# Kernel optimization log

Measured on AMD Instinct MI355X. Metric: run time of the kernel, lower is better.

## Reference

```python
import jax, jax.numpy as jnp
import numpy as np
import math

EMBED_DIM = 768
NUM_HEADS = 12
SEQ_LEN = 2048
NUM_BLOCKS = 8
BLOCK_SIZE = EMBED_DIM // NUM_BLOCKS  # 96
HEAD_DIM = EMBED_DIM // NUM_HEADS     # 64
BATCH = 4


def build_sparse_mask(T):
    # local window of 5 (j in [i-4, i]) plus log-stride links at i-8, i-16, ...
    m = np.full((T, T), -np.inf, dtype=np.float32)
    for i in range(T):
        for j in range(max(0, i - 4), i + 1):
            m[i, j] = 0.0
        step = 8
        while i - step >= 0:
            m[i, i - step] = 0.0
            step *= 2
    return jnp.asarray(m)


def make_urdhva_params(key):
    k1, k2, k3 = jax.random.split(key, 3)
    s = BLOCK_SIZE ** 0.5
    Wv = jax.random.normal(k1, (NUM_BLOCKS, BLOCK_SIZE, BLOCK_SIZE), jnp.float32) / s
    Wr = jax.random.normal(k2, (NUM_BLOCKS - 1, BLOCK_SIZE, BLOCK_SIZE), jnp.float32) / s
    Wl = jax.random.normal(k3, (NUM_BLOCKS - 1, BLOCK_SIZE, BLOCK_SIZE), jnp.float32) / s
    b = jnp.zeros((EMBED_DIM,), jnp.float32)
    return Wv, Wr, Wl, b


def urdhva_linear(x, Wv, Wr, Wl, b):
    # x: [..., EMBED_DIM] -> block-diagonal + neighbor cross-block linear
    shp = x.shape
    xb = x.reshape(-1, NUM_BLOCKS, BLOCK_SIZE)  # [N, B, S]
    y = jnp.einsum('nbs,bst->nbt', xb, Wv)
    y = y.at[:, 1:, :].add(jnp.einsum('nbs,bst->nbt', xb[:, :-1, :], Wr))
    y = y.at[:, :-1, :].add(jnp.einsum('nbs,bst->nbt', xb[:, 1:, :], Wl))
    return y.reshape(shp) + b


def setup_inputs() -> dict:
    key = jax.random.key(0)
    kx, kq, kk, kv, ko = jax.random.split(key, 5)
    inp = {'x': jax.random.normal(kx, (BATCH, SEQ_LEN, EMBED_DIM), jnp.float32)}
    for name, k in (('q', kq), ('k', kk), ('v', kv), ('o', ko)):
        Wv, Wr, Wl, b = make_urdhva_params(k)
        inp[name + '_Wv'] = Wv
        inp[name + '_Wr'] = Wr
        inp[name + '_Wl'] = Wl
        inp[name + '_b'] = b
    inp['sparse_mask'] = build_sparse_mask(SEQ_LEN)
    return inp


def reference(x, q_Wv, q_Wr, q_Wl, q_b, k_Wv, k_Wr, k_Wl, k_b,
              v_Wv, v_Wr, v_Wl, v_b, o_Wv, o_Wr, o_Wl, o_b, sparse_mask):
    B, T, C = x.shape
    H, D = NUM_HEADS, HEAD_DIM
    q = urdhva_linear(x, q_Wv, q_Wr, q_Wl, q_b).reshape(B, T, H, D).transpose(0, 2, 1, 3)
    k = urdhva_linear(x, k_Wv, k_Wr, k_Wl, k_b).reshape(B, T, H, D).transpose(0, 2, 1, 3)
    v = urdhva_linear(x, v_Wv, v_Wr, v_Wl, v_b).reshape(B, T, H, D).transpose(0, 2, 1, 3)
    scores = jnp.einsum('bhqd,bhkd->bhqk', q, k) / math.sqrt(D)
    scores = scores + sparse_mask[:T, :T]
    attn = jax.nn.softmax(scores, axis=-1)
    out = jnp.einsum('bhqk,bhkd->bhqd', attn, v).transpose(0, 2, 1, 3).reshape(B, T, C)
    return urdhva_linear(out, o_Wv, o_Wr, o_Wl, o_b)
```

## Files before the change

kernel.cpp:

```cpp
#include <hip/hip_runtime.h>
#include <hip/hip_bf16.h>

typedef __hip_bfloat16 bf16;
typedef __attribute__((ext_vector_type(8))) short short8;
typedef __attribute__((ext_vector_type(4))) float f32x4;

#define ED 768
#define NB 8
#define BS 96
#define NH 12
#define HD 64
#define SEQ 2048
#define NBATCH 4
#define NROWS (NBATCH*SEQ)

__device__ __forceinline__ float b2f(bf16 v){ return __bfloat162float(v); }
__device__ __forceinline__ bf16 f2b(float v){ return __float2bfloat16(v); }
__device__ __forceinline__ short f2bs(float v){
    return (short)__builtin_bit_cast(unsigned short, __float2bfloat16(v));
}
__device__ __forceinline__ unsigned pkbf16(float lo, float hi){
    return (unsigned)(unsigned short)f2bs(lo) |
           ((unsigned)(unsigned short)f2bs(hi) << 16);
}
__device__ __forceinline__ void gload_lds16(const void* g, void* l) {
    __builtin_amdgcn_global_load_lds(
        (const __attribute__((address_space(1))) unsigned*)g,
        (__attribute__((address_space(3))) unsigned*)l, 16, 0, 0);
}

#define XCVT_BLKS (NROWS*ED/8/256)
#define DENS_BLKS (ED*ED/256)
__global__ __launch_bounds__(256) void prep(
    const float* __restrict__ x, bf16* __restrict__ xb,
    const float* __restrict__ qWv, const float* __restrict__ qWr, const float* __restrict__ qWl,
    const float* __restrict__ kWv, const float* __restrict__ kWr, const float* __restrict__ kWl,
    const float* __restrict__ vWv, const float* __restrict__ vWr, const float* __restrict__ vWl,
    const float* __restrict__ oWv, const float* __restrict__ oWr, const float* __restrict__ oWl,
    bf16* __restrict__ WdBase)
{
    if (blockIdx.x < XCVT_BLKS) {
        const int idx = blockIdx.x*256 + threadIdx.x;
        const float4 a = ((const float4*)x)[(size_t)idx*2];
        const float4 c = ((const float4*)x)[(size_t)idx*2 + 1];
        short8 o;
        o[0]=f2bs(a.x); o[1]=f2bs(a.y); o[2]=f2bs(a.z); o[3]=f2bs(a.w);
        o[4]=f2bs(c.x); o[5]=f2bs(c.y); o[6]=f2bs(c.z); o[7]=f2bs(c.w);
        ((short8*)xb)[idx] = o;
    } else {
        const int bid = blockIdx.x - XCVT_BLKS;
        const int z = bid / DENS_BLKS;
        const float* Wv = (z==0)?qWv:(z==1)?kWv:(z==2)?vWv:oWv;
        const float* Wr = (z==0)?qWr:(z==1)?kWr:(z==2)?vWr:oWr;
        const float* Wl = (z==0)?qWl:(z==1)?kWl:(z==2)?vWl:oWl;
        bf16* Wd = WdBase + (size_t)z*ED*ED;

        const int idx = (bid - z*DENS_BLKS)*256 + threadIdx.x;
        const int t = idx / ED, s = idx - t*ED;
        const int bt = t / BS, tt = t - bt*BS;
        const int bs = s / BS, ss = s - bs*BS;
        float val = 0.f;
        if (bs == bt)        val = Wv[(bt*BS + ss)*BS + tt];
        else if (bs == bt-1) val = Wr[((bt-1)*BS + ss)*BS + tt];
        else if (bs == bt+1) val = Wl[(bt*BS + ss)*BS + tt];
        Wd[idx] = f2b(val);
    }
}

__device__ __forceinline__ void stage64(
    const bf16* __restrict__ Ag, const bf16* __restrict__ Wd,
    int rowbase, int colbase, int k0,
    bf16* As, bf16* Bs, int wave, int lane)
{
    const int r8 = lane >> 3;
    const int sl = lane & 7;
    const int kofs = ((sl ^ r8) << 3);
    #pragma unroll
    for (int c = wave; c < 28; c += 4) {
        if (c < 16) {
            const int row = c*8 + r8;
            gload_lds16(Ag + (size_t)(rowbase + row)*ED + k0 + kofs,
                        (char*)As + c*1024);
        } else {
            const int row = (c-16)*8 + r8;
            gload_lds16(Wd + (size_t)(colbase + row)*ED + k0 + kofs,
                        (char*)Bs + (c-16)*1024);
        }
    }
}

__device__ __forceinline__ void compute64(
    const bf16* As, const bf16* Bs, int wave, int lane, f32x4 acc[2][6])
{
    const int l15 = lane & 15;
    const int s   = lane >> 4;
    #pragma unroll
    for (int ks = 0; ks < 2; ++ks) {
        short8 a[2], b[6];
        #pragma unroll
        for (int rf = 0; rf < 2; ++rf) {
            const int row = wave*32 + rf*16 + l15;
            a[rf] = *(const short8*)((const char*)As + row*128 +
                        ((((ks<<2)+s) ^ (row&7)) << 4));
        }
        #pragma unroll
        for (int nf = 0; nf < 6; ++nf) {
            const int row = nf*16 + l15;
            b[nf] = *(const short8*)((const char*)Bs + row*128 +
                        ((((ks<<2)+s) ^ (row&7)) << 4));
        }
        #pragma unroll
        for (int rf = 0; rf < 2; ++rf)
            #pragma unroll
            for (int nf = 0; nf < 6; ++nf)
                acc[rf][nf] = __builtin_amdgcn_mfma_f32_16x16x32_bf16(
                                  a[rf], b[nf], acc[rf][nf], 0, 0, 0);
    }
}

__device__ __forceinline__ void stage32(
    const bf16* __restrict__ Ag, const bf16* __restrict__ Wd,
    int rowbase, int colbase, int k0,
    bf16* As, bf16* Bs, int wave, int lane)
{
    const int sub  = lane >> 2;
    const int slot = lane & 3;
    const int sws  = ((lane >> 2) ^ (lane >> 4)) & 3;
    const int kofs = ((slot ^ sws) << 3);
    #pragma unroll
    for (int c = wave; c < 14; c += 4) {
        if (c < 8) {
            const int r = c*16 + sub;
            gload_lds16(Ag + (size_t)(rowbase + r)*ED + k0 + kofs,
                        (char*)As + c*1024);
        } else {
            const int col = (c-8)*16 + sub;
            gload_lds16(Wd + (size_t)(colbase + col)*ED + k0 + kofs,
                        (char*)Bs + (c-8)*1024);
        }
    }
}

__device__ __forceinline__ void compute32(
    const bf16* As, const bf16* Bs, int wave, int lane, f32x4 acc[2][6])
{
    const int l15 = lane & 15;
    const int s   = lane >> 4;
    const int swr = (l15 ^ (l15 >> 2)) & 3;
    const int rsel = ((s ^ swr) << 4);

    short8 a[2], b[6];
    #pragma unroll
    for (int rf = 0; rf < 2; ++rf)
        a[rf] = *(const short8*)((const char*)As +
                    (wave*32 + rf*16 + l15)*64 + rsel);
    #pragma unroll
    for (int nf = 0; nf < 6; ++nf)
        b[nf] = *(const short8*)((const char*)Bs + (nf*16 + l15)*64 + rsel);
    #pragma unroll
    for (int rf = 0; rf < 2; ++rf)
        #pragma unroll
        for (int nf = 0; nf < 6; ++nf)
            acc[rf][nf] = __builtin_amdgcn_mfma_f32_16x16x32_bf16(
                              a[rf], b[nf], acc[rf][nf], 0, 0, 0);
}

template<bool OBF16>
__global__ __launch_bounds__(256, 2) void urdhva_gemm_lds(
    const bf16* __restrict__ A,
    const bf16* __restrict__ WdBase,
    const float* __restrict__ bias0, const float* __restrict__ bias1,
    const float* __restrict__ bias2,
    void* __restrict__ OutBase)
{
    __shared__ __align__(16) bf16 As[2][128*64];
    __shared__ __align__(16) bf16 Bs[2][96*64];

    const int z = blockIdx.z;
    const bf16* Wd = WdBase + (size_t)z*ED*ED;
    const float* bias = (z==0) ? bias0 : (z==1) ? bias1 : bias2;

    const int lane = threadIdx.x & 63;
    const int wave = threadIdx.x >> 6;
    const int rowbase = blockIdx.x*128;
    const int ob = blockIdx.y;
    const int colbase = ob*BS;
    const int klo = (ob==0)    ? 0  : (ob-1)*BS;
    const int khi = (ob==NB-1) ? ED : (ob+2)*BS;
    const int band = khi - klo;
    const int nt64 = band >> 6;
    const bool tail = (band & 63) != 0;

    f32x4 acc[2][6];
    #pragma unroll
    for (int i=0;i<2;++i)
        #pragma unroll
        for (int j=0;j<6;++j) acc[i][j] = (f32x4){0.f,0.f,0.f,0.f};

    stage64(A, Wd, rowbase, colbase, klo, As[0], Bs[0], wave, lane);
    __syncthreads();
    int cur = 0;
    for (int t = 1; t < nt64; ++t) {
        stage64(A, Wd, rowbase, colbase, klo + t*64,
                As[cur^1], Bs[cur^1], wave, lane);
        compute64(As[cur], Bs[cur], wave, lane, acc);
        __syncthreads();
        cur ^= 1;
    }
    if (tail) {
        stage32(A, Wd, rowbase, colbase, klo + nt64*64,
                As[cur^1], Bs[cur^1], wave, lane);
        compute64(As[cur], Bs[cur], wave, lane, acc);
        __syncthreads();
        cur ^= 1;
        compute32(As[cur], Bs[cur], wave, lane, acc);
    } else {
        compute64(As[cur], Bs[cur], wave, lane, acc);
    }

    const int l15 = lane & 15;
    const int rbase = (lane >> 4) * 4;
    const int wrow = rowbase + wave*32;
    if (OBF16 && z == 2) {
        bf16* vT = (bf16*)OutBase + (size_t)2*NROWS*ED;
        #pragma unroll
        for (int rf = 0; rf < 2; ++rf) {
            #pragma unroll
            for (int nf = 0; nf < 6; ++nf) {
                const int col = colbase + nf*16 + l15;
                const float bv = bias[col];
                const int row0 = wrow + rf*16 + rbase;
                uint2 dw;
                dw.x = pkbf16(acc[rf][nf][0] + bv, acc[rf][nf][1] + bv);
                dw.y = pkbf16(acc[rf][nf][2] + bv, acc[rf][nf][3] + bv);
                *(uint2*)(vT + ((size_t)(row0 >> 4)*ED + col)*16 + (row0 & 15)) = dw;
            }
        }
    } else {
        #pragma unroll
        for (int rf = 0; rf < 2; ++rf) {
            #pragma unroll
            for (int nf = 0; nf < 6; ++nf) {
                const int col = colbase + nf*16 + l15;
                const float bv = bias[col];
                #pragma unroll
                for (int r = 0; r < 4; ++r) {
                    const int row = wrow + rf*16 + rbase + r;
                    const float vv = acc[rf][nf][r] + bv;
                    if (OBF16)
                        ((bf16*)OutBase)[(size_t)z*NROWS*ED + (size_t)row*ED + col] = f2b(vv);
                    else
                        ((float*)OutBase)[(size_t)row*ED + col] = vv;
                }
            }
        }
    }
}

__global__ __launch_bounds__(256) void sparse_attn_mfma(
    const bf16* __restrict__ q, const bf16* __restrict__ k,
    const bf16* __restrict__ vT, bf16* __restrict__ out)
{
    __shared__ __align__(16) char shm[24*16*128];

    const int lane = threadIdx.x & 63;
    const int wid  = threadIdx.x >> 6;
    const int o   = (blockIdx.x & 7)*192 + (blockIdx.x >> 3);
    const int hb  = o >> 5;
    const int qt0 = (o & 31) << 2;
    const int h   = hb % NH;
    const int bb  = hb / NH;
    const int I   = qt0 << 4;
    const int i0  = I + (wid << 4);

    const int l15 = lane & 15;
    const int g   = lane >> 4;

    const bf16* qbase = q + ((size_t)bb*SEQ + i0 + l15)*ED + h*HD + g*8;
    const short8 qf0 = *(const short8*)qbase;
    const short8 qf1 = *(const short8*)(qbase + 32);

    int bases[8];
    bases[0]=i0;     bases[1]=i0-16;  bases[2]=i0-32;  bases[3]=i0-64;
    bases[4]=i0-128; bases[5]=i0-256; bases[6]=i0-512; bases[7]=i0-1024;

    short8 vfrag[4][4];
    #pragma unroll
    for (int u = 0; u < 4; ++u) {
        const int tb = (g & 2) ? bases[2*u+1] : bases[2*u];
        const size_t gt = (size_t)bb*128 + ((tb < 0 ? 0 : tb) >> 4);
        #pragma unroll
        for (int nt = 0; nt < 4; ++nt)
            vfrag[u][nt] = *(const short8*)(vT +
                (gt*ED + h*HD + 16*nt + l15)*16 + 8*(g & 1));
    }

    const bf16* kbb = k + (size_t)bb*SEQ*ED + h*HD;
    #pragma unroll
    for (int c = 0; c < 12; ++c) {
        const int id  = c*256 + threadIdx.x;
        const int row = id >> 3;
        const int sl  = id & 7;
        const int j   = row >> 4;
        int tb;
        if (j < 8) tb = I + 48 - (j << 4);
        else       tb = I + (((j-8) >> 2) << 4) - (128 << ((j-8) & 3));
        const int gr = (tb < 0 ? 0 : tb) + (row & 15);
        gload_lds16(kbb + (size_t)gr*ED + ((sl ^ (row & 7)) << 3),
                    shm + id*16);
    }
    __syncthreads();

    float p[8][4];
    #pragma unroll
    for (int t = 0; t < 8; ++t) {
        const int j = (t < 4) ? ((t == 3 ? 7 : 3 + t) - wid)
                              : (8 + 4*wid + (t - 4));
        f32x4 acc = (f32x4){0.f,0.f,0.f,0.f};
        if (bases[t] >= 0) {
            const char* kr = shm + (j*16 + l15)*128;
            const int sw = l15 & 7;
            const short8 kf0 = *(const short8*)(kr + ((g ^ sw) << 4));
            const short8 kf1 = *(const short8*)(kr + (((g+4) ^ sw) << 4));
            acc = __builtin_amdgcn_mfma_f32_16x16x32_bf16(kf0, qf0, acc, 0,0,0);
            acc = __builtin_amdgcn_mfma_f32_16x16x32_bf16(kf1, qf1, acc, 0,0,0);
        }
        const int Dt = i0 - bases[t];
        #pragma unroll
        for (int r = 0; r < 4; ++r) {
            const int delta = Dt + l15 - 4*g - r;
            const bool val = (bases[t] >= 0) &&
                (((unsigned)delta <= 4u) ||
                 (delta >= 8 && (delta & (delta-1)) == 0));
            p[t][r] = val ? acc[r]*0.125f : -1e30f;
        }
    }

    float m = -1e30f;
    #pragma unroll
    for (int t = 0; t < 8; ++t)
        #pragma unroll
        for (int r = 0; r < 4; ++r) m = fmaxf(m, p[t][r]);
    m = fmaxf(m, __shfl_xor(m, 16));
    m = fmaxf(m, __shfl_xor(m, 32));

    float den = 0.f;
    #pragma unroll
    for (int t = 0; t < 8; ++t)
        #pragma unroll
        for (int r = 0; r < 4; ++r) { p[t][r] = __expf(p[t][r] - m); den += p[t][r]; }
    den += __shfl_xor(den, 16);
    den += __shfl_xor(den, 32);
    const float inv = 1.f / den;

    __syncthreads();

    {
        char* prow = shm + wid*4352 + l15*272;
        #pragma unroll
        for (int t = 0; t < 8; ++t) {
            *(unsigned*)(prow + 32*t + 8*g)     = pkbf16(p[t][0]*inv, p[t][1]*inv);
            *(unsigned*)(prow + 32*t + 8*g + 4) = pkbf16(p[t][2]*inv, p[t][3]*inv);
        }
    }

    f32x4 accO[4];
    #pragma unroll
    for (int nt = 0; nt < 4; ++nt) accO[nt] = (f32x4){0.f,0.f,0.f,0.f};

    #pragma unroll
    for (int u = 0; u < 4; ++u) {
        const short8 pa = *(const short8*)(shm + wid*4352 + l15*272 + 64*u + 16*g);
        #pragma unroll
        for (int nt = 0; nt < 4; ++nt)
            accO[nt] = __builtin_amdgcn_mfma_f32_16x16x32_bf16(
                           pa, vfrag[u][nt], accO[nt], 0,0,0);
    }

    #pragma unroll
    for (int nt = 0; nt < 4; ++nt)
        #pragma unroll
        for (int r = 0; r < 4; ++r)
            out[((size_t)bb*SEQ + i0 + 4*g + r)*ED + h*HD + 16*nt + l15] =
                f2b(accO[nt][r]);
}

extern "C" void kernel_launch(void* const* d_in, const int* in_sizes, int n_in,
                              void* d_out, int out_size, void* d_ws, size_t ws_size,
                              hipStream_t stream) {
    const float* x   = (const float*)d_in[0];
    const float* qWv = (const float*)d_in[1];
    const float* qWr = (const float*)d_in[2];
    const float* qWl = (const float*)d_in[3];
    const float* qb  = (const float*)d_in[4];
    const float* kWv = (const float*)d_in[5];
    const float* kWr = (const float*)d_in[6];
    const float* kWl = (const float*)d_in[7];
    const float* kb  = (const float*)d_in[8];
    const float* vWv = (const float*)d_in[9];
    const float* vWr = (const float*)d_in[10];
    const float* vWl = (const float*)d_in[11];
    const float* vb  = (const float*)d_in[12];
    const float* oWv = (const float*)d_in[13];
    const float* oWr = (const float*)d_in[14];
    const float* oWl = (const float*)d_in[15];
    const float* ob  = (const float*)d_in[16];

    const size_t QKV = (size_t)NROWS*ED;
    bf16* xb  = (bf16*)d_ws;
    bf16* q   = xb + QKV;
    bf16* k   = q + QKV;
    bf16* vT  = k + QKV;
    bf16* ao  = vT + QKV;
    bf16* Wd  = ao + QKV;
    bf16* Wdo = Wd + (size_t)3*ED*ED;

    prep<<<XCVT_BLKS + 4*DENS_BLKS, 256, 0, stream>>>(
        x, xb,
        qWv,qWr,qWl, kWv,kWr,kWl, vWv,vWr,vWl, oWv,oWr,oWl, Wd);

    urdhva_gemm_lds<true><<<dim3(NROWS/128, NB, 3), 256, 0, stream>>>(
        xb, Wd, qb, kb, vb, q);

    sparse_attn_mfma<<<(NBATCH*NH*(SEQ/16))/4, 256, 0, stream>>>(q, k, vT, ao);

    urdhva_gemm_lds<false><<<dim3(NROWS/128, NB, 1), 256, 0, stream>>>(
        ao, Wdo, ob, ob, ob, d_out);
}
```

Measured before the change: 68.04 us.

## Fuse x fp32-to-bf16 conversion into a single QKV GEMM sharing the A tile

Drops the separate x-to-bf16 pass and xb buffer. The QKV GEMM now loads fp32 x directly, converts it in registers and writes it to LDS. One block computes Q, K and V for its row/column tile, so each A tile is loaded once instead of three times across the z dimension. The cost is a 3x larger accumulator set (72 f32x4 per thread), which adds register pressure and may lower occupancy, and a smaller K step of 32 per stage.

```diff
diff --git a/kernel.cpp b/kernel.cpp
--- a/kernel.cpp
+++ b/kernel.cpp
@@ -29,42 +29,165 @@
         (__attribute__((address_space(3))) unsigned*)l, 16, 0, 0);
 }
 
-#define XCVT_BLKS (NROWS*ED/8/256)
-#define DENS_BLKS (ED*ED/256)
-__global__ __launch_bounds__(256) void prep(
-    const float* __restrict__ x, bf16* __restrict__ xb,
+__global__ __launch_bounds__(256) void densify4(
     const float* __restrict__ qWv, const float* __restrict__ qWr, const float* __restrict__ qWl,
     const float* __restrict__ kWv, const float* __restrict__ kWr, const float* __restrict__ kWl,
     const float* __restrict__ vWv, const float* __restrict__ vWr, const float* __restrict__ vWl,
     const float* __restrict__ oWv, const float* __restrict__ oWr, const float* __restrict__ oWl,
     bf16* __restrict__ WdBase)
 {
-    if (blockIdx.x < XCVT_BLKS) {
-        const int idx = blockIdx.x*256 + threadIdx.x;
-        const float4 a = ((const float4*)x)[(size_t)idx*2];
-        const float4 c = ((const float4*)x)[(size_t)idx*2 + 1];
-        short8 o;
-        o[0]=f2bs(a.x); o[1]=f2bs(a.y); o[2]=f2bs(a.z); o[3]=f2bs(a.w);
-        o[4]=f2bs(c.x); o[5]=f2bs(c.y); o[6]=f2bs(c.z); o[7]=f2bs(c.w);
-        ((short8*)xb)[idx] = o;
-    } else {
-        const int bid = blockIdx.x - XCVT_BLKS;
-        const int z = bid / DENS_BLKS;
-        const float* Wv = (z==0)?qWv:(z==1)?kWv:(z==2)?vWv:oWv;
-        const float* Wr = (z==0)?qWr:(z==1)?kWr:(z==2)?vWr:oWr;
-        const float* Wl = (z==0)?qWl:(z==1)?kWl:(z==2)?vWl:oWl;
-        bf16* Wd = WdBase + (size_t)z*ED*ED;
-
-        const int idx = (bid - z*DENS_BLKS)*256 + threadIdx.x;
-        const int t = idx / ED, s = idx - t*ED;
-        const int bt = t / BS, tt = t - bt*BS;
-        const int bs = s / BS, ss = s - bs*BS;
-        float val = 0.f;
-        if (bs == bt)        val = Wv[(bt*BS + ss)*BS + tt];
-        else if (bs == bt-1) val = Wr[((bt-1)*BS + ss)*BS + tt];
-        else if (bs == bt+1) val = Wl[(bt*BS + ss)*BS + tt];
-        Wd[idx] = f2b(val);
-    }
+    const int z = blockIdx.y;
+    const float* Wv = (z==0)?qWv:(z==1)?kWv:(z==2)?vWv:oWv;
+    const float* Wr = (z==0)?qWr:(z==1)?kWr:(z==2)?vWr:oWr;
+    const float* Wl = (z==0)?qWl:(z==1)?kWl:(z==2)?vWl:oWl;
+    bf16* Wd = WdBase + (size_t)z*ED*ED;
+
+    const int idx = blockIdx.x*256 + threadIdx.x;
+    const int t = idx / ED, s = idx - t*ED;
+    const int bt = t / BS, tt = t - bt*BS;
+    const int bs = s / BS, ss = s - bs*BS;
+    float val = 0.f;
+    if (bs == bt)        val = Wv[(bt*BS + ss)*BS + tt];
+    else if (bs == bt-1) val = Wr[((bt-1)*BS + ss)*BS + tt];
+    else if (bs == bt+1) val = Wl[(bt*BS + ss)*BS + tt];
+    Wd[idx] = f2b(val);
+}
+
+__global__ __launch_bounds__(256, 2) void qkv_gemm_fused(
+    const float* __restrict__ x,
+    const bf16* __restrict__ WdBase,
+    const float* __restrict__ qb, const float* __restrict__ kb,
+    const float* __restrict__ vb,
+    bf16* __restrict__ qo, bf16* __restrict__ ko, bf16* __restrict__ vT)
+{
+    __shared__ __align__(16) bf16 As[2][128*32];
+    __shared__ __align__(16) bf16 Bs[2][3*96*32];
+
+    const int tid  = threadIdx.x;
+    const int lane = tid & 63;
+    const int wave = tid >> 6;
+    const int rowbase = blockIdx.x*128;
+    const int ob = blockIdx.y;
+    const int colbase = ob*BS;
+    const int klo = (ob==0)    ? 0  : (ob-1)*BS;
+    const int khi = (ob==NB-1) ? ED : (ob+2)*BS;
+    const int nt  = (khi - klo) >> 5;
+
+    const int ar  = tid >> 1;
+    const int ah  = tid & 1;
+    const int asw = ((ar & 15) ^ ((ar & 15) >> 2)) & 3;
+    const int as0 = ((2*ah)   ^ asw) << 4;
+    const int as1 = ((2*ah+1) ^ asw) << 4;
+    const float* axbase = x + (size_t)(rowbase + ar)*ED + 16*ah;
+
+    const int sub  = lane >> 2;
+    const int slot = lane & 3;
+    const int sws  = (sub ^ (sub >> 2)) & 3;
+    const int kofs = ((slot ^ sws) << 3);
+
+    f32x4 acc[3][2][6];
+    #pragma unroll
+    for (int z=0;z<3;++z)
+        #pragma unroll
+        for (int i=0;i<2;++i)
+            #pragma unroll
+            for (int j=0;j<6;++j) acc[z][i][j] = (f32x4){0.f,0.f,0.f,0.f};
+
+    float4 fr0, fr1, fr2, fr3;
+    #define STAGE_A_LOAD(K0) do { \
+        const float* ap = axbase + (K0); \
+        fr0 = *(const float4*)ap; fr1 = *(const float4*)(ap+4); \
+        fr2 = *(const float4*)(ap+8); fr3 = *(const float4*)(ap+12); } while(0)
+
+    #define STAGE_A_WRITE(BUF) do { \
+        short8 lo, hi; \
+        lo[0]=f2bs(fr0.x); lo[1]=f2bs(fr0.y); lo[2]=f2bs(fr0.z); lo[3]=f2bs(fr0.w); \
+        lo[4]=f2bs(fr1.x); lo[5]=f2bs(fr1.y); lo[6]=f2bs(fr1.z); lo[7]=f2bs(fr1.w); \
+        hi[0]=f2bs(fr2.x); hi[1]=f2bs(fr2.y); hi[2]=f2bs(fr2.z); hi[3]=f2bs(fr2.w); \
+        hi[4]=f2bs(fr3.x); hi[5]=f2bs(fr3.y); hi[6]=f2bs(fr3.z); hi[7]=f2bs(fr3.w); \
+        char* abase = (char*)(BUF) + ar*64; \
+        *(short8*)(abase + as0) = lo; \
+        *(short8*)(abase + as1) = hi; } while(0)
+
+    #define STAGE_B(K0, BUF) do { \
+        _Pragma("unroll") \
+        for (int zz = 0; zz < 3; ++zz) \
+            for (int c = wave; c < 6; c += 4) { \
+                const int r = c*16 + sub; \
+                gload_lds16(WdBase + (size_t)zz*ED*ED + \
+                            (size_t)(colbase + r)*ED + (K0) + kofs, \
+                            (char*)(BUF) + zz*6144 + c*1024); \
+            } } while(0)
+
+    STAGE_A_LOAD(klo);
+    STAGE_B(klo, Bs[0]);
+    STAGE_A_WRITE(As[0]);
+    __syncthreads();
+
+    const int l15 = lane & 15;
+    const int s   = lane >> 4;
+    const int swr = (l15 ^ (l15 >> 2)) & 3;
+    const int rsel = ((s ^ swr) << 4);
+
+    #define COMPUTE(BUFA, BUFB) do { \
+        short8 a0 = *(const short8*)((const char*)(BUFA) + (wave*32 + l15)*64 + rsel); \
+        short8 a1 = *(const short8*)((const char*)(BUFA) + (wave*32 + 16 + l15)*64 + rsel); \
+        _Pragma("unroll") \
+        for (int zz = 0; zz < 3; ++zz) { \
+            short8 b[6]; \
+            _Pragma("unroll") \
+            for (int nf = 0; nf < 6; ++nf) \
+                b[nf] = *(const short8*)((const char*)(BUFB) + zz*6144 + \
+                            (nf*16 + l15)*64 + rsel); \
+            _Pragma("unroll") \
+            for (int nf = 0; nf < 6; ++nf) { \
+                acc[zz][0][nf] = __builtin_amdgcn_mfma_f32_16x16x32_bf16(a0, b[nf], acc[zz][0][nf], 0,0,0); \
+                acc[zz][1][nf] = __builtin_amdgcn_mfma_f32_16x16x32_bf16(a1, b[nf], acc[zz][1][nf], 0,0,0); \
+            } } } while(0)
+
+    int cur = 0;
+    for (int t = 0; t < nt-1; ++t) {
+        STAGE_A_LOAD(klo + (t+1)*32);
+        STAGE_B(klo + (t+1)*32, Bs[cur^1]);
+        COMPUTE(As[cur], Bs[cur]);
+        STAGE_A_WRITE(As[cur^1]);
+        __syncthreads();
+        cur ^= 1;
+    }
+    COMPUTE(As[cur], Bs[cur]);
+
+    const int rbase = (lane >> 4) * 4;
+    const int wrow = rowbase + wave*32;
+    #pragma unroll
+    for (int zz = 0; zz < 3; ++zz) {
+        const float* bias = (zz==0) ? qb : (zz==1) ? kb : vb;
+        #pragma unroll
+        for (int rf = 0; rf < 2; ++rf) {
+            #pragma unroll
+            for (int nf = 0; nf < 6; ++nf) {
+                const int col = colbase + nf*16 + l15;
+                const float bv = bias[col];
+                if (zz == 2) {
+                    const int row0 = wrow + rf*16 + rbase;
+                    uint2 dw;
+                    dw.x = pkbf16(acc[2][rf][nf][0] + bv, acc[2][rf][nf][1] + bv);
+                    dw.y = pkbf16(acc[2][rf][nf][2] + bv, acc[2][rf][nf][3] + bv);
+                    *(uint2*)(vT + ((size_t)(row0 >> 4)*ED + col)*16 + (row0 & 15)) = dw;
+                } else {
+                    bf16* outp = (zz==0) ? qo : ko;
+                    #pragma unroll
+                    for (int r = 0; r < 4; ++r) {
+                        const int row = wrow + rf*16 + rbase + r;
+                        outp[(size_t)row*ED + col] = f2b(acc[zz][rf][nf][r] + bv);
+                    }
+                }
+            }
+        }
+    }
+    #undef STAGE_A_LOAD
+    #undef STAGE_A_WRITE
+    #undef STAGE_B
+    #undef COMPUTE
 }
 
 __device__ __forceinline__ void stage64(
@@ -118,14 +241,14 @@
     }
 }
 
-__device__ __forceinline__ void stage32(
+__device__ __forceinline__ void stage32o(
     const bf16* __restrict__ Ag, const bf16* __restrict__ Wd,
     int rowbase, int colbase, int k0,
     bf16* As, bf16* Bs, int wave, int lane)
 {
     const int sub  = lane >> 2;
     const int slot = lane & 3;
-    const int sws  = ((lane >> 2) ^ (lane >> 4)) & 3;
+    const int sws  = (sub ^ (sub >> 2)) & 3;
     const int kofs = ((slot ^ sws) << 3);
     #pragma unroll
     for (int c = wave; c < 14; c += 4) {
@@ -141,7 +264,7 @@
     }
 }
 
-__device__ __forceinline__ void compute32(
+__device__ __forceinline__ void compute32o(
     const bf16* As, const bf16* Bs, int wave, int lane, f32x4 acc[2][6])
 {
     const int l15 = lane & 15;
@@ -165,20 +288,14 @@
                               a[rf], b[nf], acc[rf][nf], 0, 0, 0);
 }
 
-template<bool OBF16>
-__global__ __launch_bounds__(256, 2) void urdhva_gemm_lds(
+__global__ __launch_bounds__(256, 2) void o_gemm_lds(
     const bf16* __restrict__ A,
-    const bf16* __restrict__ WdBase,
-    const float* __restrict__ bias0, const float* __restrict__ bias1,
-    const float* __restrict__ bias2,
-    void* __restrict__ OutBase)
+    const bf16* __restrict__ Wd,
+    const float* __restrict__ bias,
+    float* __restrict__ Out)
 {
     __shared__ __align__(16) bf16 As[2][128*64];
     __shared__ __align__(16) bf16 Bs[2][96*64];
-
-    const int z = blockIdx.z;
-    const bf16* Wd = WdBase + (size_t)z*ED*ED;
-    const float* bias = (z==0) ? bias0 : (z==1) ? bias1 : bias2;
 
     const int lane = threadIdx.x & 63;
     const int wave = threadIdx.x >> 6;
@@ -208,12 +325,12 @@
         cur ^= 1;
     }
     if (tail) {
-        stage32(A, Wd, rowbase, colbase, klo + nt64*64,
-                As[cur^1], Bs[cur^1], wave, lane);
+        stage32o(A, Wd, rowbase, colbase, klo + nt64*64,
+                 As[cur^1], Bs[cur^1], wave, lane);
         compute64(As[cur], Bs[cur], wave, lane, acc);
         __syncthreads();
         cur ^= 1;
-        compute32(As[cur], Bs[cur], wave, lane, acc);
+        compute32o(As[cur], Bs[cur], wave, lane, acc);
     } else {
         compute64(As[cur], Bs[cur], wave, lane, acc);
     }
@@ -221,37 +338,16 @@
     const int l15 = lane & 15;
     const int rbase = (lane >> 4) * 4;
     const int wrow = rowbase + wave*32;
-    if (OBF16 && z == 2) {
-        bf16* vT = (bf16*)OutBase + (size_t)2*NROWS*ED;
-        #pragma unroll
-        for (int rf = 0; rf < 2; ++rf) {
+    #pragma unroll
+    for (int rf = 0; rf < 2; ++rf) {
+        #pragma unroll
+        for (int nf = 0; nf < 6; ++nf) {
+            const int col = colbase + nf*16 + l15;
+            const float bv = bias[col];
             #pragma unroll
-            for (int nf = 0; nf < 6; ++nf) {
-                const int col = colbase + nf*16 + l15;
-                const float bv = bias[col];
-                const int row0 = wrow + rf*16 + rbase;
-                uint2 dw;
-                dw.x = pkbf16(acc[rf][nf][0] + bv, acc[rf][nf][1] + bv);
-                dw.y = pkbf16(acc[rf][nf][2] + bv, acc[rf][nf][3] + bv);
-                *(uint2*)(vT + ((size_t)(row0 >> 4)*ED + col)*16 + (row0 & 15)) = dw;
-            }
-        }
-    } else {
-        #pragma unroll
-        for (int rf = 0; rf < 2; ++rf) {
-            #pragma unroll
-            for (int nf = 0; nf < 6; ++nf) {
-                const int col = colbase + nf*16 + l15;
-                const float bv = bias[col];
-                #pragma unroll
-                for (int r = 0; r < 4; ++r) {
-                    const int row = wrow + rf*16 + rbase + r;
-                    const float vv = acc[rf][nf][r] + bv;
-                    if (OBF16)
-                        ((bf16*)OutBase)[(size_t)z*NROWS*ED + (size_t)row*ED + col] = f2b(vv);
-                    else
-                        ((float*)OutBase)[(size_t)row*ED + col] = vv;
-                }
+            for (int r = 0; r < 4; ++r) {
+                const int row = wrow + rf*16 + rbase + r;
+                Out[(size_t)row*ED + col] = acc[rf][nf][r] + bv;
             }
         }
     }
@@ -407,23 +503,20 @@
     const float* ob  = (const float*)d_in[16];
 
     const size_t QKV = (size_t)NROWS*ED;
-    bf16* xb  = (bf16*)d_ws;
-    bf16* q   = xb + QKV;
+    bf16* q   = (bf16*)d_ws;
     bf16* k   = q + QKV;
     bf16* vT  = k + QKV;
     bf16* ao  = vT + QKV;
     bf16* Wd  = ao + QKV;
     bf16* Wdo = Wd + (size_t)3*ED*ED;
 
-    prep<<<XCVT_BLKS + 4*DENS_BLKS, 256, 0, stream>>>(
-        x, xb,
+    densify4<<<dim3(ED*ED/256, 4), 256, 0, stream>>>(
         qWv,qWr,qWl, kWv,kWr,kWl, vWv,vWr,vWl, oWv,oWr,oWl, Wd);
 
-    urdhva_gemm_lds<true><<<dim3(NROWS/128, NB, 3), 256, 0, stream>>>(
-        xb, Wd, qb, kb, vb, q);
+    qkv_gemm_fused<<<dim3(NROWS/128, NB), 256, 0, stream>>>(
+        x, Wd, qb, kb, vb, q, k, vT);
 
     sparse_attn_mfma<<<(NBATCH*NH*(SEQ/16))/4, 256, 0, stream>>>(q, k, vT, ao);
 
-    urdhva_gemm_lds<false><<<dim3(NROWS/128, NB, 1), 256, 0, stream>>>(
-        ao, Wdo, ob, ob, ob, d_out);
-}
+    o_gemm_lds<<<dim3(NROWS/128, NB), 256, 0, stream>>>(ao, Wdo, ob, (float*)d_out);
+}
```

Result: faster. 63.59 us (-6.6%).
